# Kernel tuning notes

Hardware: AMD Instinct MI355X
Metric: run time of the kernel (lower is better)

The kernel has to match this reference:

```python
import jax, jax.numpy as jnp
import numpy as np

EPS = 1e-4  # BatchNorm2d eps from source


def binarize(x):
    # brevitas 1-bit quant: sign(x) with sign(0)=+1; straight-through (clipped) estimator
    y = jnp.clip(x, -1.0, 1.0)
    q = jnp.where(x >= 0, 1.0, -1.0).astype(x.dtype)
    return y + jax.lax.stop_gradient(q - y)


def bn(x, g, b, m, v):
    inv = g / jnp.sqrt(v + EPS)
    return x * inv[None, :, None, None] + (b - m * inv)[None, :, None, None]


def conv(x, w, pad):
    return jax.lax.conv_general_dilated(
        x, w, window_strides=(1, 1), padding=[(pad, pad), (pad, pad)],
        dimension_numbers=('NCHW', 'OIHW', 'NCHW'))


def conv_mod(x, w1, bn1, w3, bn3):
    # conv1x1(binary W) -> BN -> binarize act -> conv3x3(binary W) -> BN -> binarize act
    x = conv(x, binarize(w1), 0)
    x = binarize(bn(x, *bn1))
    x = conv(x, binarize(w3), 1)
    x = binarize(bn(x, *bn3))
    return x


def maxpool2(x):
    return jax.lax.reduce_window(x, -jnp.inf, jax.lax.max,
                                 (1, 1, 2, 2), (1, 1, 2, 2), 'VALID')


def setup_inputs() -> dict:
    key = jax.random.key(0)
    ks = jax.random.split(key, 24)
    B, Cin, down, up, H, W = 16, 256, 64, 256, 56, 56
    d = {
        'x':   jax.random.normal(ks[0], (B, Cin, H, W), jnp.float32),
        'w11': jax.random.normal(ks[1], (down, Cin, 1, 1), jnp.float32) * 0.1,
        'w31': jax.random.normal(ks[2], (up, down, 3, 3), jnp.float32) * 0.1,
        'w12': jax.random.normal(ks[3], (down, up, 1, 1), jnp.float32) * 0.1,
        'w32': jax.random.normal(ks[4], (up, down, 3, 3), jnp.float32) * 0.1,
    }
    # BatchNorm params (inference stats): gamma, beta, running mean, running var
    for i, (tag, c) in enumerate([('11', down), ('31', up), ('12', down), ('32', up)]):
        d['g' + tag] = jax.random.uniform(ks[5 + 4 * i], (c,), jnp.float32, 0.5, 1.5)
        d['b' + tag] = jax.random.normal(ks[6 + 4 * i], (c,), jnp.float32) * 0.1
        d['m' + tag] = jax.random.normal(ks[7 + 4 * i], (c,), jnp.float32) * 0.1
        d['v' + tag] = jax.random.uniform(ks[8 + 4 * i], (c,), jnp.float32, 0.5, 1.5)
    return d


def reference(x, w11, w31, w12, w32,
              g11, b11, m11, v11, g31, b31, m31, v31,
              g12, b12, m12, v12, g32, b32, m32, v32):
    h = conv_mod(x, w11, (g11, b11, m11, v11), w31, (g31, b31, m31, v31))
    r = conv_mod(h, w12, (g12, b12, m12, v12), w32, (g32, b32, m32, v32))
    s = binarize(h + r)          # quant_add: re-binarize the residual sum
    return maxpool2(s)           # MaxPool2d(2)
```

## Files before the change

kernel.cpp:

```cpp
#include <hip/hip_runtime.h>
#include <stdint.h>

#pragma clang fp contract(off)


#define HW_   3136
#define NPIX  50176

#define OFF_W31B   0
#define OFF_W12B   18432
#define OFF_W32B   20480
#define OFF_IV11   38912
#define OFF_IV31   39424
#define OFF_IV12   41472
#define OFF_IV32   41984
#define OFF_SGNT   44032
#define OFF_A1     109568
#define OFF_A2     510976
#define OFF_H      912384
#define OFF_S      2518016

__device__ inline float2 mk_ivbt(float g, float b, float m, float v) {
    float inv  = __fdiv_rn(g, __fsqrt_rn(__fadd_rn(v, 1e-4f)));
    float beta = __fsub_rn(b, __fmul_rn(m, inv));
    return make_float2(inv, beta);
}

__global__ __launch_bounds__(256) void k0_all(
    const float* __restrict__ w11, const float* __restrict__ w31,
    const float* __restrict__ w12, const float* __restrict__ w32,
    const float* __restrict__ g11, const float* __restrict__ b11,
    const float* __restrict__ m11, const float* __restrict__ v11,
    const float* __restrict__ g31, const float* __restrict__ b31,
    const float* __restrict__ m31, const float* __restrict__ v31,
    const float* __restrict__ g12, const float* __restrict__ b12,
    const float* __restrict__ m12, const float* __restrict__ v12,
    const float* __restrict__ g32, const float* __restrict__ b32,
    const float* __restrict__ m32, const float* __restrict__ v32,
    uint64_t* __restrict__ W31b, uint64_t* __restrict__ W12b,
    uint64_t* __restrict__ W32b,
    float2* __restrict__ iv11, float2* __restrict__ iv31,
    float2* __restrict__ iv12, float2* __restrict__ iv32,
    float* __restrict__ sgnT)
{
    int blk = blockIdx.x;
    if (blk < 1216) {
        int wid = blk * 4 + (threadIdx.x >> 6);
        int l = threadIdx.x & 63;
        if (wid < 2304) {
            int co = wid / 9, tap = wid % 9;
            uint64_t bits = __ballot(w31[(co * 64 + l) * 9 + tap] >= 0.f);
            if (l == 0) W31b[wid] = bits;
        } else if (wid < 4608) {
            int i = wid - 2304;
            int co = i / 9, tap = i % 9;
            uint64_t bits = __ballot(w32[(co * 64 + l) * 9 + tap] >= 0.f);
            if (l == 0) W32b[i] = bits;
        } else if (wid < 4864) {
            int i = wid - 4608;
            int co = i >> 2, k = i & 3;
            uint64_t bits = __ballot(w12[co * 256 + k * 64 + l] >= 0.f);
            if (l == 0) W12b[i] = bits;
        }
    } else if (blk < 1219) {
        int i = (blk - 1216) * 256 + threadIdx.x;
        if (i < 64)        iv11[i]       = mk_ivbt(g11[i],       b11[i],       m11[i],       v11[i]);
        else if (i < 320)  iv31[i - 64]  = mk_ivbt(g31[i - 64],  b31[i - 64],  m31[i - 64],  v31[i - 64]);
        else if (i < 384)  iv12[i - 320] = mk_ivbt(g12[i - 320], b12[i - 320], m12[i - 320], v12[i - 320]);
        else if (i < 640)  iv32[i - 384] = mk_ivbt(g32[i - 384], b32[i - 384], m32[i - 384], v32[i - 384]);
    } else {
        int t = (blk - 1219) * 256 + threadIdx.x;
        int j = t >> 8, ci = t & 255;
        sgnT[ci * 64 + j] = (w11[t] >= 0.f) ? 1.0f : -1.0f;
    }
}

__global__ __launch_bounds__(512) void k1_conv1(
    const float* __restrict__ x, const float* __restrict__ sgnT,
    const float2* __restrict__ ivbt, unsigned char* __restrict__ A1)
{
    const int l = threadIdx.x & 63;
    const int g = __builtin_amdgcn_readfirstlane(threadIdx.x >> 6);
    const int P = blockIdx.x * 256 + l * 4;
    const int bl = P / HW_;
    const int pxl = P - bl * HW_;
    const float* xp = x + (size_t)bl * (256 * HW_) + pxl;
    const float* sg = sgnT + g * 8;

    float acc[8][4];
#pragma unroll
    for (int j = 0; j < 8; ++j)
#pragma unroll
        for (int p = 0; p < 4; ++p) acc[j][p] = 0.0f;

    for (int ci = 0; ci < 256; ci += 8) {
        float4 xv[8];
#pragma unroll
        for (int k = 0; k < 8; ++k)
            xv[k] = *(const float4*)(xp + (size_t)(ci + k) * HW_);
#pragma unroll
        for (int k = 0; k < 8; ++k) {
            const float* s = sg + (ci + k) * 64;
#pragma unroll
            for (int j = 0; j < 8; ++j) {
                acc[j][0] = __builtin_fmaf(s[j], xv[k].x, acc[j][0]);
                acc[j][1] = __builtin_fmaf(s[j], xv[k].y, acc[j][1]);
                acc[j][2] = __builtin_fmaf(s[j], xv[k].z, acc[j][2]);
                acc[j][3] = __builtin_fmaf(s[j], xv[k].w, acc[j][3]);
            }
        }
    }

    unsigned bp0 = 0, bp1 = 0, bp2 = 0, bp3 = 0;
#pragma unroll
    for (int j = 0; j < 8; ++j) {
        float2 ib = ivbt[g * 8 + j];
        bp0 |= (__fadd_rn(__fmul_rn(acc[j][0], ib.x), ib.y) >= 0.0f) ? (1u << j) : 0u;
        bp1 |= (__fadd_rn(__fmul_rn(acc[j][1], ib.x), ib.y) >= 0.0f) ? (1u << j) : 0u;
        bp2 |= (__fadd_rn(__fmul_rn(acc[j][2], ib.x), ib.y) >= 0.0f) ? (1u << j) : 0u;
        bp3 |= (__fadd_rn(__fmul_rn(acc[j][3], ib.x), ib.y) >= 0.0f) ? (1u << j) : 0u;
    }
    unsigned char* a = A1 + (size_t)P * 8 + g;
    a[0]  = (unsigned char)bp0;
    a[8]  = (unsigned char)bp1;
    a[16] = (unsigned char)bp2;
    a[24] = (unsigned char)bp3;
}

template <bool MERGE>
__global__ __launch_bounds__(256) void k_conv3b(
    const uint64_t* __restrict__ A, const uint64_t* __restrict__ Wb,
    const float2* __restrict__ ivbt, const uint64_t* __restrict__ Hin,
    uint64_t* __restrict__ Out)
{
    __shared__ uint64_t tile[4 * 58];
    const int l = threadIdx.x & 63;
    const int wv = threadIdx.x >> 6;
    const int chunk = blockIdx.x;
    const int b = chunk / 49;
    const int hw0 = (chunk % 49) * 64;
    const int r0 = hw0 / 56;
    const int o  = hw0 % 56;
    const int rfirst = r0 - 1;

    {
        int idx = threadIdx.x;
        if (idx < 4 * 58) {
            int rr = idx / 58, cc = idx % 58;
            int gh = rfirst + rr, gw = cc - 1;
            uint64_t v = 0;
            if ((unsigned)gh < 56u && (unsigned)gw < 56u)
                v = A[b * HW_ + gh * 56 + gw];
            tile[idx] = v;
        }
    }

    const int co = wv * 64 + l;
    uint64_t wp[9];
    int c64[9];
#pragma unroll
    for (int t = 0; t < 9; ++t) {
        wp[t] = Wb[co * 9 + t];
        c64[t] = 64 - 2 * (int)__popcll(wp[t]);
    }
    const float2 ib = ivbt[co];

    __syncthreads();

    uint64_t res = 0;
    for (int p = 0; p < 64; ++p) {
        const int inrow2 = (p >= 56 - o) ? 1 : 0;
        const int w = o + p - (inrow2 ? 56 : 0);
        const int row = r0 + inrow2;
        const int rbase = inrow2 * 58;

        int s = 0;
#pragma unroll
        for (int dr = 0; dr < 3; ++dr)
#pragma unroll
            for (int dc = 0; dc < 3; ++dc) {
                uint64_t a = tile[rbase + dr * 58 + w + dc];
                s += (int)__popcll(a ^ wp[dr * 3 + dc]);
            }
        int y = 576 - 2 * s;

        unsigned um = 0;
        if (row == 0)  um |= 0x007u;
        if (row == 55) um |= 0x1C0u;
        if (w == 0)    um |= 0x049u;
        if (w == 55)   um |= 0x124u;
        if (um) {
#pragma unroll
            for (int t = 0; t < 9; ++t)
                if ((um >> t) & 1u) y -= c64[t];
        }

        float val = __fadd_rn(__fmul_rn((float)y, ib.x), ib.y);
        uint64_t word = __ballot(val >= 0.0f);
        res = (l == p) ? word : res;
    }

    size_t oidx = (size_t)wv * NPIX + (size_t)(b * HW_) + hw0 + l;
    if (MERGE) res |= Hin[oidx];
    Out[oidx] = res;
}

__global__ __launch_bounds__(256) void k3_conv1b(
    const uint64_t* __restrict__ H, const uint64_t* __restrict__ W12b,
    const float2* __restrict__ ivbt, uint64_t* __restrict__ A2)
{
    int p = blockIdx.x * 256 + threadIdx.x;
    uint64_t h0 = H[p];
    uint64_t h1 = H[NPIX + p];
    uint64_t h2 = H[2 * NPIX + p];
    uint64_t h3 = H[3 * NPIX + p];
    uint64_t bits = 0;
#pragma unroll 4
    for (int co = 0; co < 64; ++co) {
        const uint64_t* wp = W12b + co * 4;
        int s = (int)(__popcll(h0 ^ wp[0]) + __popcll(h1 ^ wp[1]) +
                      __popcll(h2 ^ wp[2]) + __popcll(h3 ^ wp[3]));
        int y = 256 - 2 * s;
        float2 ib = ivbt[co];
        float val = __fadd_rn(__fmul_rn((float)y, ib.x), ib.y);
        bits |= (uint64_t)(val >= 0.0f) << co;
    }
    A2[p] = bits;
}

__global__ __launch_bounds__(256) void k4b_pool(
    const uint64_t* __restrict__ S, float* __restrict__ out)
{
    int o = blockIdx.x * 256 + threadIdx.x;
    int ow = o % 28;
    int t = o / 28;
    int oh = t % 28; t /= 28;
    int co = t & 255;
    int b  = t >> 8;
    int k = co >> 6, j = co & 63;
    const uint64_t* Sk = S + (size_t)k * NPIX + (size_t)(b * HW_) + (2 * oh) * 56 + 2 * ow;
    uint64_t s = Sk[0] | Sk[1] | Sk[56] | Sk[57];
    out[o] = ((s >> j) & 1) ? 1.0f : -1.0f;
}

extern "C" void kernel_launch(void* const* d_in, const int* in_sizes, int n_in,
                              void* d_out, int out_size, void* d_ws, size_t ws_size,
                              hipStream_t stream)
{
    const float* x   = (const float*)d_in[0];
    const float* w11 = (const float*)d_in[1];
    const float* w31 = (const float*)d_in[2];
    const float* w12 = (const float*)d_in[3];
    const float* w32 = (const float*)d_in[4];
    const float* g11 = (const float*)d_in[5];
    const float* b11 = (const float*)d_in[6];
    const float* m11 = (const float*)d_in[7];
    const float* v11 = (const float*)d_in[8];
    const float* g31 = (const float*)d_in[9];
    const float* b31 = (const float*)d_in[10];
    const float* m31 = (const float*)d_in[11];
    const float* v31 = (const float*)d_in[12];
    const float* g12 = (const float*)d_in[13];
    const float* b12 = (const float*)d_in[14];
    const float* m12 = (const float*)d_in[15];
    const float* v12 = (const float*)d_in[16];
    const float* g32 = (const float*)d_in[17];
    const float* b32 = (const float*)d_in[18];
    const float* m32 = (const float*)d_in[19];
    const float* v32 = (const float*)d_in[20];

    char* ws = (char*)d_ws;
    uint64_t* W31b = (uint64_t*)(ws + OFF_W31B);
    uint64_t* W12b = (uint64_t*)(ws + OFF_W12B);
    uint64_t* W32b = (uint64_t*)(ws + OFF_W32B);
    float2* iv11 = (float2*)(ws + OFF_IV11);
    float2* iv31 = (float2*)(ws + OFF_IV31);
    float2* iv12 = (float2*)(ws + OFF_IV12);
    float2* iv32 = (float2*)(ws + OFF_IV32);
    float*  sgnT = (float*)(ws + OFF_SGNT);
    uint64_t* A1 = (uint64_t*)(ws + OFF_A1);
    uint64_t* A2 = (uint64_t*)(ws + OFF_A2);
    uint64_t* Hb = (uint64_t*)(ws + OFF_H);
    uint64_t* Sb = (uint64_t*)(ws + OFF_S);

    k0_all<<<dim3(1283), dim3(256), 0, stream>>>(
        w11, w31, w12, w32,
        g11, b11, m11, v11, g31, b31, m31, v31,
        g12, b12, m12, v12, g32, b32, m32, v32,
        W31b, W12b, W32b, iv11, iv31, iv12, iv32, sgnT);

    k1_conv1<<<dim3(196), dim3(512), 0, stream>>>(x, sgnT, iv11, (unsigned char*)A1);

    k_conv3b<false><<<dim3(784), dim3(256), 0, stream>>>(A1, W31b, iv31, (const uint64_t*)nullptr, Hb);

    k3_conv1b<<<dim3(196), dim3(256), 0, stream>>>(Hb, W12b, iv12, A2);

    k_conv3b<true><<<dim3(784), dim3(256), 0, stream>>>(A2, W32b, iv32, Hb, Sb);

    k4b_pool<<<dim3(12544), dim3(256), 0, stream>>>(Sb, (float*)d_out);
}
```

Measured before the change: 129.4 us.

## Fuse binary 1x1 conv into first 3x3 conv epilogue and split conv1 blocks

The separate k3_conv1b kernel is removed. Its popcount-based 1x1 binary convolution now runs in the epilogue of the first conv3x3 kernel: each wave shares its 64-bit output words through LDS and computes 16 of the 64 output channels. This saves a kernel launch and a re-read of H from global memory, at the cost of one extra __syncthreads and more work per block. Separately, conv1 is relaunched as 392 blocks of 256 threads, each handling half the channel groups, instead of 196 blocks of 512, to improve occupancy and scheduling.

```diff
diff --git a/kernel.cpp b/kernel.cpp
--- a/kernel.cpp
+++ b/kernel.cpp
@@ -75,13 +75,16 @@
     }
 }
 
-__global__ __launch_bounds__(512) void k1_conv1(
+__global__ __launch_bounds__(256) void k1_conv1(
     const float* __restrict__ x, const float* __restrict__ sgnT,
     const float2* __restrict__ ivbt, unsigned char* __restrict__ A1)
 {
     const int l = threadIdx.x & 63;
-    const int g = __builtin_amdgcn_readfirstlane(threadIdx.x >> 6);
-    const int P = blockIdx.x * 256 + l * 4;
+    const int wv = __builtin_amdgcn_readfirstlane(threadIdx.x >> 6);
+    const int blk = blockIdx.x;
+    const int half = blk & 1;
+    const int g = half * 4 + wv;
+    const int P = (blk >> 1) * 256 + l * 4;
     const int bl = P / HW_;
     const int pxl = P - bl * HW_;
     const float* xp = x + (size_t)bl * (256 * HW_) + pxl;
@@ -127,13 +130,16 @@
     a[24] = (unsigned char)bp3;
 }
 
-template <bool MERGE>
+template <bool MERGE, bool DO_K3>
 __global__ __launch_bounds__(256) void k_conv3b(
     const uint64_t* __restrict__ A, const uint64_t* __restrict__ Wb,
     const float2* __restrict__ ivbt, const uint64_t* __restrict__ Hin,
-    uint64_t* __restrict__ Out)
+    uint64_t* __restrict__ Out,
+    const uint64_t* __restrict__ W12b, const float2* __restrict__ iv12,
+    unsigned short* __restrict__ A2)
 {
     __shared__ uint64_t tile[4 * 58];
+    __shared__ uint64_t sh4[4][64];
     const int l = threadIdx.x & 63;
     const int wv = threadIdx.x >> 6;
     const int chunk = blockIdx.x;
@@ -203,29 +209,25 @@
     size_t oidx = (size_t)wv * NPIX + (size_t)(b * HW_) + hw0 + l;
     if (MERGE) res |= Hin[oidx];
     Out[oidx] = res;
-}
-
-__global__ __launch_bounds__(256) void k3_conv1b(
-    const uint64_t* __restrict__ H, const uint64_t* __restrict__ W12b,
-    const float2* __restrict__ ivbt, uint64_t* __restrict__ A2)
-{
-    int p = blockIdx.x * 256 + threadIdx.x;
-    uint64_t h0 = H[p];
-    uint64_t h1 = H[NPIX + p];
-    uint64_t h2 = H[2 * NPIX + p];
-    uint64_t h3 = H[3 * NPIX + p];
-    uint64_t bits = 0;
-#pragma unroll 4
-    for (int co = 0; co < 64; ++co) {
-        const uint64_t* wp = W12b + co * 4;
-        int s = (int)(__popcll(h0 ^ wp[0]) + __popcll(h1 ^ wp[1]) +
-                      __popcll(h2 ^ wp[2]) + __popcll(h3 ^ wp[3]));
-        int y = 256 - 2 * s;
-        float2 ib = ivbt[co];
-        float val = __fadd_rn(__fmul_rn((float)y, ib.x), ib.y);
-        bits |= (uint64_t)(val >= 0.0f) << co;
-    }
-    A2[p] = bits;
+
+    if (DO_K3) {
+        sh4[wv][l] = res;
+        __syncthreads();
+        uint64_t h0 = sh4[0][l], h1 = sh4[1][l], h2 = sh4[2][l], h3 = sh4[3][l];
+        unsigned bits16 = 0;
+#pragma unroll
+        for (int jj = 0; jj < 16; ++jj) {
+            int cq = wv * 16 + jj;
+            const uint64_t* wq = W12b + cq * 4;
+            int s = (int)(__popcll(h0 ^ wq[0]) + __popcll(h1 ^ wq[1]) +
+                          __popcll(h2 ^ wq[2]) + __popcll(h3 ^ wq[3]));
+            int y = 256 - 2 * s;
+            float2 ibq = iv12[cq];
+            float val = __fadd_rn(__fmul_rn((float)y, ibq.x), ibq.y);
+            bits16 |= (val >= 0.0f) ? (1u << jj) : 0u;
+        }
+        A2[(size_t)(b * HW_ + hw0 + l) * 4 + wv] = (unsigned short)bits16;
+    }
 }
 
 __global__ __launch_bounds__(256) void k4b_pool(
@@ -289,13 +291,15 @@
         g12, b12, m12, v12, g32, b32, m32, v32,
         W31b, W12b, W32b, iv11, iv31, iv12, iv32, sgnT);
 
-    k1_conv1<<<dim3(196), dim3(512), 0, stream>>>(x, sgnT, iv11, (unsigned char*)A1);
-
-    k_conv3b<false><<<dim3(784), dim3(256), 0, stream>>>(A1, W31b, iv31, (const uint64_t*)nullptr, Hb);
-
-    k3_conv1b<<<dim3(196), dim3(256), 0, stream>>>(Hb, W12b, iv12, A2);
-
-    k_conv3b<true><<<dim3(784), dim3(256), 0, stream>>>(A2, W32b, iv32, Hb, Sb);
+    k1_conv1<<<dim3(392), dim3(256), 0, stream>>>(x, sgnT, iv11, (unsigned char*)A1);
+
+    k_conv3b<false, true><<<dim3(784), dim3(256), 0, stream>>>(
+        A1, W31b, iv31, (const uint64_t*)nullptr, Hb,
+        W12b, iv12, (unsigned short*)A2);
+
+    k_conv3b<true, false><<<dim3(784), dim3(256), 0, stream>>>(
+        A2, W32b, iv32, Hb, Sb,
+        (const uint64_t*)nullptr, (const float2*)nullptr, (unsigned short*)nullptr);
 
     k4b_pool<<<dim3(12544), dim3(256), 0, stream>>>(Sb, (float*)d_out);
 }
```

Result: faster. 120.2 us (-7.1%).
